# Kernel tuning notes

Measured on AMD Instinct MI355X. Metric: run time of the kernel, lower is better.

## Reference

```python
import jax, jax.numpy as jnp
import numpy as np
import math

D_MODEL = 256
N_LEVELS = 4
N_HEADS = 8
N_POINTS = 4
SPATIAL = [[92, 160], [46, 80], [23, 40], [12, 20]]  # (H_l, W_l)
BATCH = 8
LEN_Q = 8192


def setup_inputs() -> dict:
    key = jax.random.key(0)
    ks = jax.random.split(key, 8)
    len_in = sum(h * w for h, w in SPATIAL)
    query = jax.random.normal(ks[0], (BATCH, LEN_Q, D_MODEL), jnp.float32)
    reference_points = jax.random.uniform(ks[1], (BATCH, LEN_Q, N_LEVELS, 2), jnp.float32)
    input_flatten = jax.random.normal(ks[2], (BATCH, len_in, D_MODEL), jnp.float32)
    input_spatial_shapes = jnp.array(SPATIAL, jnp.int32)
    starts = np.cumsum([0] + [h * w for h, w in SPATIAL])[:-1]
    input_level_start_index = jnp.array(starts, jnp.int32)
    # learned params (sampling_offsets bias uses the directional grid init from _reset_parameters)
    W_off = jax.random.normal(ks[3], (D_MODEL, N_HEADS * N_LEVELS * N_POINTS * 2), jnp.float32) * 0.01
    thetas = jnp.arange(N_HEADS, dtype=jnp.float32) * (2.0 * math.pi / N_HEADS)
    grid = jnp.stack([jnp.cos(thetas), jnp.sin(thetas)], -1)
    grid = grid / jnp.max(jnp.abs(grid), axis=-1, keepdims=True)
    grid = jnp.tile(grid[:, None, None, :], (1, N_LEVELS, N_POINTS, 1))
    grid = grid * jnp.arange(1, N_POINTS + 1, dtype=jnp.float32)[None, None, :, None]
    b_off = grid.reshape(-1)
    W_attn = jax.random.normal(ks[4], (D_MODEL, N_HEADS * N_LEVELS * N_POINTS), jnp.float32) * 0.02
    b_attn = jnp.zeros((N_HEADS * N_LEVELS * N_POINTS,), jnp.float32)
    W_val = jax.random.normal(ks[5], (D_MODEL, D_MODEL), jnp.float32) * (1.0 / math.sqrt(D_MODEL))
    b_val = jnp.zeros((D_MODEL,), jnp.float32)
    W_out = jax.random.normal(ks[6], (D_MODEL, D_MODEL), jnp.float32) * (1.0 / math.sqrt(D_MODEL))
    b_out = jnp.zeros((D_MODEL,), jnp.float32)
    return dict(query=query, reference_points=reference_points, input_flatten=input_flatten,
                input_spatial_shapes=input_spatial_shapes,
                input_level_start_index=input_level_start_index,
                W_off=W_off, b_off=b_off, W_attn=W_attn, b_attn=b_attn,
                W_val=W_val, b_val=b_val, W_out=W_out, b_out=b_out)


def _ms_deform_attn(query, reference_points, input_flatten, spatial_shapes_np,
                    W_off, b_off, W_attn, b_attn, W_val, b_val, W_out, b_out):
    Nb, Lq, C = query.shape
    Hh, L, P = N_HEADS, N_LEVELS, N_POINTS
    Dh = C // Hh
    value = (input_flatten @ W_val + b_val).reshape(Nb, -1, Hh, Dh)
    attn = (query @ W_attn + b_attn).reshape(Nb, Lq, Hh, L * P)
    attn = jax.nn.softmax(attn, axis=-1).reshape(Nb, Lq, Hh, L, P)
    off = (query @ W_off + b_off).reshape(Nb, Lq, Hh, L, P, 2)
    # offset_normalizer = (W_l, H_l)
    norm = jnp.asarray(np.stack([spatial_shapes_np[:, 1], spatial_shapes_np[:, 0]], -1),
                       dtype=query.dtype)  # (L, 2)
    loc = reference_points[:, :, None, :, None, :] + off / norm[None, None, None, :, None, :]
    out = jnp.zeros((Nb, Lq, Hh, Dh), query.dtype)
    start = 0
    for l in range(L):
        H, W = int(spatial_shapes_np[l, 0]), int(spatial_shapes_np[l, 1])
        v = value[:, start:start + H * W]                       # (Nb, H*W, Hh, Dh)
        start += H * W
        v = v.transpose(0, 2, 1, 3).reshape(Nb * Hh, H * W, Dh)  # (B2, H*W, Dh)
        g = loc[:, :, :, l].transpose(0, 2, 1, 3, 4).reshape(Nb * Hh, Lq * P, 2)
        # grid_sample with grid = 2*loc-1, align_corners=False, zero padding
        x = g[..., 0] * W - 0.5
        y = g[..., 1] * H - 0.5
        x0f = jnp.floor(x); y0f = jnp.floor(y)
        wx = x - x0f; wy = y - y0f
        x0 = x0f.astype(jnp.int32); y0 = y0f.astype(jnp.int32)

        def gather(xi, yi):
            valid = (xi >= 0) & (xi < W) & (yi >= 0) & (yi < H)
            idx = jnp.clip(yi, 0, H - 1) * W + jnp.clip(xi, 0, W - 1)
            samp = jnp.take_along_axis(v, idx[..., None], axis=1)  # (B2, Lq*P, Dh)
            return samp * valid[..., None].astype(v.dtype)

        s = (gather(x0, y0) * ((1 - wx) * (1 - wy))[..., None]
             + gather(x0 + 1, y0) * (wx * (1 - wy))[..., None]
             + gather(x0, y0 + 1) * ((1 - wx) * wy)[..., None]
             + gather(x0 + 1, y0 + 1) * (wx * wy)[..., None])
        s = s.reshape(Nb, Hh, Lq, P, Dh)
        w = attn[:, :, :, l].transpose(0, 2, 1, 3)  # (Nb, Hh, Lq, P)
        out = out + jnp.einsum('bhqp,bhqpd->bqhd', w, s)
    return out.reshape(Nb, Lq, C) @ W_out + b_out


def reference(query, reference_points, input_flatten, input_spatial_shapes,
              input_level_start_index, W_off, b_off, W_attn, b_attn,
              W_val, b_val, W_out, b_out):
    # spatial shapes are static metadata (define per-level view sizes)
    shapes_np = np.asarray(input_spatial_shapes)
    del input_level_start_index  # levels are contiguous; starts derived from shapes
    return _ms_deform_attn(query, reference_points, input_flatten, shapes_np,
                           W_off, b_off, W_attn, b_attn, W_val, b_val, W_out, b_out)
```

## Files before the change

### kernel.cpp

```cpp
#include <hip/hip_runtime.h>
#include <hip/hip_bf16.h>
#include <cstddef>
#include <cstdint>

#define NB 8
#define LQ 8192
#define DMODEL 256
#define NHD 8
#define NLV 4
#define NPT 4
#define LEN_IN 19560
#define NQ (NB * LQ)
#define MV (NB * LEN_IN)
#define MVP 156544

using bf16x8 = __attribute__((ext_vector_type(8))) short;
using f32x4  = __attribute__((ext_vector_type(4))) float;

typedef const __attribute__((address_space(1))) void* gas_ptr;
typedef __attribute__((address_space(3))) void* las_ptr;

__device__ __forceinline__ void gl_lds16(const void* g, void* l) {
  __builtin_amdgcn_global_load_lds((gas_ptr)g, (las_ptr)l, 16, 0, 0);
}
__device__ __forceinline__ float bflo(unsigned u) {
  union { unsigned i; float f; } c; c.i = u << 16; return c.f;
}
__device__ __forceinline__ float bfhi(unsigned u) {
  union { unsigned i; float f; } c; c.i = u & 0xffff0000u; return c.f;
}
__device__ __forceinline__ bf16x8 pack8(float4 a, float4 b) {
  bf16x8 o;
  o[0] = (short)__bfloat16_as_ushort(__float2bfloat16(a.x));
  o[1] = (short)__bfloat16_as_ushort(__float2bfloat16(a.y));
  o[2] = (short)__bfloat16_as_ushort(__float2bfloat16(a.z));
  o[3] = (short)__bfloat16_as_ushort(__float2bfloat16(a.w));
  o[4] = (short)__bfloat16_as_ushort(__float2bfloat16(b.x));
  o[5] = (short)__bfloat16_as_ushort(__float2bfloat16(b.y));
  o[6] = (short)__bfloat16_as_ushort(__float2bfloat16(b.z));
  o[7] = (short)__bfloat16_as_ushort(__float2bfloat16(b.w));
  return o;
}

__global__ __launch_bounds__(256) void transpose_bf16(
    const float* __restrict__ W, __hip_bfloat16* __restrict__ Bt, int N) {
  const int o = blockIdx.x * 256 + threadIdx.x;
  const int n = o >> 8, k = o & 255;
  Bt[o] = __float2bfloat16(W[(size_t)k * N + n]);
}

template <int OUT_MODE, int A_F32>
__global__ __launch_bounds__(256) void gemm_mfma(
    const void* __restrict__ Av, const __hip_bfloat16* __restrict__ Bt,
    const float* __restrict__ bias, const float* __restrict__ bias2,
    void* __restrict__ Cout, void* __restrict__ Cout2, int N, int M_valid) {
  __shared__ __hip_bfloat16 As[128 * 32];
  __shared__ __hip_bfloat16 Bs[128 * 32];

  const int tid = threadIdx.x;
  const int wv = tid >> 6;
  const int lane = tid & 63;
  const int quad = lane >> 4;
  const int l16 = lane & 15;
  const int bm = blockIdx.y * 128;
  const int bn = blockIdx.x * 128;
  const int rw = (wv & 1) * 64;
  const int cw = (wv >> 1) * 64;

  const __hip_bfloat16* gB = Bt + (size_t)(bn + (tid >> 2)) * 256 + (tid & 3) * 8;
  char* ldsB0 = (char*)Bs + wv * 1024;

  const __hip_bfloat16* gA16 = nullptr;
  const float* gA32 = nullptr;
  char* ldsA0 = (char*)As + wv * 1024;
  __hip_bfloat16* dA = nullptr;
  bool okA = true;
  if (A_F32) {
    const int r = tid >> 1, half = tid & 1;
    okA = (bm + r) < M_valid;
    gA32 = (const float*)Av + (size_t)(bm + r) * 256 + half * 16;
    dA = As + r * 32 + half * 16;
  } else {
    gA16 = (const __hip_bfloat16*)Av + (size_t)(bm + (tid >> 2)) * 256 +
           (tid & 3) * 8;
  }

  f32x4 acc[4][4] = {};

#pragma unroll 1
  for (int k0 = 0; k0 < 256; k0 += 32) {
    float4 f0, f1, f2, f3;
    if (A_F32) {
      if (okA) {
        f0 = *(const float4*)(gA32 + k0);
        f1 = *(const float4*)(gA32 + k0 + 4);
        f2 = *(const float4*)(gA32 + k0 + 8);
        f3 = *(const float4*)(gA32 + k0 + 12);
      } else {
        f0 = f1 = f2 = f3 = make_float4(0.f, 0.f, 0.f, 0.f);
      }
    }
    __syncthreads();
    gl_lds16(gB + k0, ldsB0);
    gl_lds16(gB + 64 * 256 + k0, ldsB0 + 4096);
    if (A_F32) {
      *(bf16x8*)dA = pack8(f0, f1);
      *(bf16x8*)(dA + 8) = pack8(f2, f3);
    } else {
      gl_lds16(gA16 + k0, ldsA0);
      gl_lds16(gA16 + 64 * 256 + k0, ldsA0 + 4096);
    }
    __syncthreads();

    bf16x8 af[4], bfr[4];
#pragma unroll
    for (int t = 0; t < 4; ++t) {
      af[t] = *(const bf16x8*)(As + (rw + t * 16 + l16) * 32 + quad * 8);
      bfr[t] = *(const bf16x8*)(Bs + (cw + t * 16 + l16) * 32 + quad * 8);
    }
#pragma unroll
    for (int i = 0; i < 4; ++i)
#pragma unroll
      for (int j = 0; j < 4; ++j)
        acc[i][j] = __builtin_amdgcn_mfma_f32_16x16x32_bf16(af[i], bfr[j],
                                                            acc[i][j], 0, 0, 0);
  }

#pragma unroll
  for (int j = 0; j < 4; ++j) {
    const int col = bn + cw + j * 16 + l16;
    float bb;
    if (OUT_MODE == 3)
      bb = (bn == 0) ? bias[col] : bias2[col - 128];
    else
      bb = bias[col];
#pragma unroll
    for (int i = 0; i < 4; ++i) {
#pragma unroll
      for (int r = 0; r < 4; ++r) {
        const int row = bm + rw + i * 16 + quad * 4 + r;
        const float v = acc[i][j][r] + bb;
        if (OUT_MODE == 0) {
          ((float*)Cout)[(size_t)row * N + col] = v;
        } else if (OUT_MODE == 2) {
          if (row < M_valid) {
            const int b = row / LEN_IN;
            const int pix = row - b * LEN_IN;
            const int h = col >> 5, ch = col & 31;
            ((__hip_bfloat16*)Cout)[(((size_t)(b * 8 + h) * LEN_IN + pix) << 5) +
                                    ch] = __float2bfloat16(v);
          }
        } else {
          if (bn == 0) {
            ((float*)Cout)[(size_t)row * 128 + col] = v;
          } else {
            ((__hip_bfloat16*)Cout2)[(size_t)row * 256 + (col - 128)] =
                __float2bfloat16(v);
          }
        }
      }
    }
  }
}

__global__ __launch_bounds__(256) void msda_sample4(
    const float* __restrict__ refp,
    const float* __restrict__ logits,
    const __hip_bfloat16* __restrict__ offb,
    const __hip_bfloat16* __restrict__ vh,
    __hip_bfloat16* __restrict__ mid) {
  const int q0 = blockIdx.x * 2;
  const int tid = threadIdx.x;

  __shared__ int2 s_d[2][8][17][4];

  {
    const int sq = tid >> 7;
    const int t = tid & 127;
    const int qg = q0 + sq;
    const int l = (t >> 2) & 3;
    constexpr int Hs[4] = {92, 46, 23, 12};
    constexpr int Ws_[4] = {160, 80, 40, 20};
    constexpr int St[4] = {0, 14720, 18400, 19320};
    const int Hl = Hs[l], Wl = Ws_[l];

    const float lg = logits[(size_t)qg * 128 + t];
    float mx = lg;
#pragma unroll
    for (int d = 1; d < 16; d <<= 1) mx = fmaxf(mx, __shfl_xor(mx, d));
    const float e = expf(lg - mx);
    float sm = e;
#pragma unroll
    for (int d = 1; d < 16; d <<= 1) sm += __shfl_xor(sm, d);
    const float w = e / sm;

    const float rx = refp[(size_t)qg * 8 + 2 * l];
    const float ry = refp[(size_t)qg * 8 + 2 * l + 1];
    const unsigned uo = *(const unsigned*)(offb + (size_t)qg * 256 + 2 * t);
    const float ox = bflo(uo), oy = bfhi(uo);

    const float x = rx * (float)Wl + ox - 0.5f;
    const float y = ry * (float)Hl + oy - 0.5f;
    const float xf = floorf(x), yf = floorf(y);
    const float wx = x - xf, wy = y - yf;
    const int x0 = (int)xf, y0 = (int)yf;
    const int x1 = x0 + 1, y1 = y0 + 1;
    const bool vx0 = (x0 >= 0) & (x0 < Wl), vx1 = (x1 >= 0) & (x1 < Wl);
    const bool vy0 = (y0 >= 0) & (y0 < Hl), vy1 = (y1 >= 0) & (y1 < Hl);
    const int cx0 = min(max(x0, 0), Wl - 1), cx1 = min(max(x1, 0), Wl - 1);
    const int cy0 = min(max(y0, 0), Hl - 1), cy1 = min(max(y1, 0), Hl - 1);

    const int o00 = (St[l] + cy0 * Wl + cx0) * 64;
    const int o01 = (St[l] + cy1 * Wl + cx0) * 64;
    const int dx = (cx1 - cx0) * 64;

    int2* dd = s_d[sq][t >> 4][t & 15];
    dd[0] = make_int2(o00,      __float_as_int((vx0 & vy0) ? w * (1.f - wx) * (1.f - wy) : 0.f));
    dd[1] = make_int2(o00 + dx, __float_as_int((vx1 & vy0) ? w * wx * (1.f - wy) : 0.f));
    dd[2] = make_int2(o01,      __float_as_int((vx0 & vy1) ? w * (1.f - wx) * wy : 0.f));
    dd[3] = make_int2(o01 + dx, __float_as_int((vx1 & vy1) ? w * wx * wy : 0.f));
  }
  __syncthreads();

  const int tap = tid & 3;
  const int cg = (tid >> 2) & 3;
  const int h = (tid >> 4) & 7;
  const int sq = tid >> 7;
  const int qg = q0 + sq;
  const int bq = q0 >> 13;

  const char* vbase = (const char*)vh + (size_t)bq * (8ULL * LEN_IN * 64);
  const int voff0 = h * (LEN_IN * 64) + cg * 16;
  const int2* sd = &s_d[sq][h][0][tap];

  float a[8] = {};
#pragma unroll
  for (int pt = 0; pt < 16; ++pt) {
    const int2 dw = sd[pt * 4];
    const float w = __int_as_float(dw.y);
    const unsigned voff = (unsigned)(voff0 + dw.x);
    const uint4 u = *(const uint4*)(vbase + voff);
    a[0] += w * bflo(u.x); a[1] += w * bfhi(u.x);
    a[2] += w * bflo(u.y); a[3] += w * bfhi(u.y);
    a[4] += w * bflo(u.z); a[5] += w * bfhi(u.z);
    a[6] += w * bflo(u.w); a[7] += w * bfhi(u.w);
  }

#pragma unroll
  for (int i = 0; i < 8; ++i) a[i] += __shfl_xor(a[i], 1);
#pragma unroll
  for (int i = 0; i < 8; ++i) a[i] += __shfl_xor(a[i], 2);

  if (tap == 0) {
    unsigned short* mp =
        (unsigned short*)mid + (size_t)qg * 256 + h * 32 + cg * 8;
    int4 o;
    o.x = (int)((unsigned)__bfloat16_as_ushort(__float2bfloat16(a[0])) |
                ((unsigned)__bfloat16_as_ushort(__float2bfloat16(a[1])) << 16));
    o.y = (int)((unsigned)__bfloat16_as_ushort(__float2bfloat16(a[2])) |
                ((unsigned)__bfloat16_as_ushort(__float2bfloat16(a[3])) << 16));
    o.z = (int)((unsigned)__bfloat16_as_ushort(__float2bfloat16(a[4])) |
                ((unsigned)__bfloat16_as_ushort(__float2bfloat16(a[5])) << 16));
    o.w = (int)((unsigned)__bfloat16_as_ushort(__float2bfloat16(a[6])) |
                ((unsigned)__bfloat16_as_ushort(__float2bfloat16(a[7])) << 16));
    *(int4*)mp = o;
  }
}

extern "C" void kernel_launch(void* const* d_in, const int* in_sizes, int n_in,
                              void* d_out, int out_size, void* d_ws,
                              size_t ws_size, hipStream_t stream) {
  const float* query = (const float*)d_in[0];
  const float* refp = (const float*)d_in[1];
  const float* inflat = (const float*)d_in[2];
  const float* W_off = (const float*)d_in[5];
  const float* b_off = (const float*)d_in[6];
  const float* W_attn = (const float*)d_in[7];
  const float* b_attn = (const float*)d_in[8];
  const float* W_val = (const float*)d_in[9];
  const float* b_val = (const float*)d_in[10];
  const float* W_out = (const float*)d_in[11];
  const float* b_out = (const float*)d_in[12];
  float* out = (float*)d_out;

  char* ws = (char*)d_ws;
  __hip_bfloat16* vh = (__hip_bfloat16*)(ws);
  float* logits = (float*)(ws + 80117760ULL);
  __hip_bfloat16* offb = (__hip_bfloat16*)(ws + 113672192ULL);
  __hip_bfloat16* mid = (__hip_bfloat16*)(ws + 147226624ULL);
  __hip_bfloat16* Btv = (__hip_bfloat16*)(ws + 180781056ULL);
  __hip_bfloat16* Btc = (__hip_bfloat16*)(ws + 180912128ULL);
  __hip_bfloat16* Btw = (__hip_bfloat16*)(ws + 181108736ULL);

  transpose_bf16<<<256, 256, 0, stream>>>(W_val, Btv, 256);
  transpose_bf16<<<128, 256, 0, stream>>>(W_attn, Btc, 128);
  transpose_bf16<<<256, 256, 0, stream>>>(W_off, Btc + 128 * 256, 256);
  transpose_bf16<<<256, 256, 0, stream>>>(W_out, Btw, 256);

  gemm_mfma<2, 1><<<dim3(2, MVP / 128), 256, 0, stream>>>(
      inflat, Btv, b_val, nullptr, vh, nullptr, 256, MV);
  gemm_mfma<3, 1><<<dim3(3, NQ / 128), 256, 0, stream>>>(
      query, Btc, b_attn, b_off, logits, offb, 384, NQ);
  msda_sample4<<<NQ / 2, 256, 0, stream>>>(refp, logits, offb, vh, mid);
  gemm_mfma<0, 0><<<dim3(2, NQ / 128), 256, 0, stream>>>(
      mid, Btw, b_out, nullptr, out, nullptr, 256, NQ);
}
```

Measured before the change: 575.0 us.

## Double-buffer GEMM LDS tiles and software-pipeline sampler gathers

The MFMA GEMM now keeps two LDS buffers per operand, so the global loads for the next K tile are issued before the current tile's MFMAs run. This hides load latency and drops one barrier per K step. The sampling kernel issues its value gathers in groups of four and prefetches the next group while accumulating the current one, to expose more memory-level parallelism. In exchange, LDS use doubles and register pressure rises, which can lower occupancy.

```diff
diff --git a/kernel.cpp b/kernel.cpp
--- a/kernel.cpp
+++ b/kernel.cpp
@@ -54,8 +54,8 @@
     const void* __restrict__ Av, const __hip_bfloat16* __restrict__ Bt,
     const float* __restrict__ bias, const float* __restrict__ bias2,
     void* __restrict__ Cout, void* __restrict__ Cout2, int N, int M_valid) {
-  __shared__ __hip_bfloat16 As[128 * 32];
-  __shared__ __hip_bfloat16 Bs[128 * 32];
+  __shared__ __hip_bfloat16 As[2][128 * 32];
+  __shared__ __hip_bfloat16 Bs[2][128 * 32];
 
   const int tid = threadIdx.x;
   const int wv = tid >> 6;
@@ -68,18 +68,18 @@
   const int cw = (wv >> 1) * 64;
 
   const __hip_bfloat16* gB = Bt + (size_t)(bn + (tid >> 2)) * 256 + (tid & 3) * 8;
-  char* ldsB0 = (char*)Bs + wv * 1024;
+  char* ldsB0 = (char*)&Bs[0][0] + wv * 1024;
 
   const __hip_bfloat16* gA16 = nullptr;
   const float* gA32 = nullptr;
-  char* ldsA0 = (char*)As + wv * 1024;
+  char* ldsA0 = (char*)&As[0][0] + wv * 1024;
   __hip_bfloat16* dA = nullptr;
   bool okA = true;
   if (A_F32) {
     const int r = tid >> 1, half = tid & 1;
     okA = (bm + r) < M_valid;
     gA32 = (const float*)Av + (size_t)(bm + r) * 256 + half * 16;
-    dA = As + r * 32 + half * 16;
+    dA = &As[0][0] + r * 32 + half * 16;
   } else {
     gA16 = (const __hip_bfloat16*)Av + (size_t)(bm + (tid >> 2)) * 256 +
            (tid & 3) * 8;
@@ -87,44 +87,87 @@
 
   f32x4 acc[4][4] = {};
 
+#define GL_B(t, buf)                                          \
+  do {                                                        \
+    gl_lds16(gB + (t) * 32, ldsB0 + (buf) * 8192);            \
+    gl_lds16(gB + 64 * 256 + (t) * 32,                        \
+             ldsB0 + (buf) * 8192 + 4096);                    \
+  } while (0)
+#define GL_A16(t, buf)                                        \
+  do {                                                        \
+    gl_lds16(gA16 + (t) * 32, ldsA0 + (buf) * 8192);          \
+    gl_lds16(gA16 + 64 * 256 + (t) * 32,                      \
+             ldsA0 + (buf) * 8192 + 4096);                    \
+  } while (0)
+#define LOADA32(t, f)                                         \
+  do {                                                        \
+    if (okA) {                                                \
+      f[0] = *(const float4*)(gA32 + (t) * 32);               \
+      f[1] = *(const float4*)(gA32 + (t) * 32 + 4);           \
+      f[2] = *(const float4*)(gA32 + (t) * 32 + 8);           \
+      f[3] = *(const float4*)(gA32 + (t) * 32 + 12);          \
+    } else {                                                  \
+      f[0] = f[1] = f[2] = f[3] = make_float4(0, 0, 0, 0);    \
+    }                                                         \
+  } while (0)
+#define PACKA(buf, f)                                         \
+  do {                                                        \
+    *(bf16x8*)(dA + (buf) * 4096) = pack8(f[0], f[1]);        \
+    *(bf16x8*)(dA + (buf) * 4096 + 8) = pack8(f[2], f[3]);    \
+  } while (0)
+#define COMPUTE(buf)                                                        \
+  do {                                                                      \
+    bf16x8 af[4], bfr[4];                                                   \
+    _Pragma("unroll") for (int t = 0; t < 4; ++t) {                         \
+      af[t] = *(const bf16x8*)(&As[0][0] + (buf) * 4096 +                   \
+                               (rw + t * 16 + l16) * 32 + quad * 8);        \
+      bfr[t] = *(const bf16x8*)(&Bs[0][0] + (buf) * 4096 +                  \
+                                (cw + t * 16 + l16) * 32 + quad * 8);       \
+    }                                                                       \
+    _Pragma("unroll") for (int i = 0; i < 4; ++i)                           \
+        _Pragma("unroll") for (int j = 0; j < 4; ++j) acc[i][j] =           \
+        __builtin_amdgcn_mfma_f32_16x16x32_bf16(af[i], bfr[j], acc[i][j],   \
+                                                0, 0, 0);                   \
+  } while (0)
+
+  {
+    float4 f[4];
+    if (A_F32) LOADA32(0, f);
+    GL_B(0, 0);
+    if (!A_F32) GL_A16(0, 0);
+    if (A_F32) PACKA(0, f);
+  }
+  __syncthreads();
+
 #pragma unroll 1
-  for (int k0 = 0; k0 < 256; k0 += 32) {
-    float4 f0, f1, f2, f3;
-    if (A_F32) {
-      if (okA) {
-        f0 = *(const float4*)(gA32 + k0);
-        f1 = *(const float4*)(gA32 + k0 + 4);
-        f2 = *(const float4*)(gA32 + k0 + 8);
-        f3 = *(const float4*)(gA32 + k0 + 12);
-      } else {
-        f0 = f1 = f2 = f3 = make_float4(0.f, 0.f, 0.f, 0.f);
-      }
+  for (int tt = 0; tt < 4; ++tt) {
+    {
+      float4 fb[4];
+      if (A_F32) LOADA32(2 * tt + 1, fb);
+      GL_B(2 * tt + 1, 1);
+      if (!A_F32) GL_A16(2 * tt + 1, 1);
+      COMPUTE(0);
+      if (A_F32) PACKA(1, fb);
     }
     __syncthreads();
-    gl_lds16(gB + k0, ldsB0);
-    gl_lds16(gB + 64 * 256 + k0, ldsB0 + 4096);
-    if (A_F32) {
-      *(bf16x8*)dA = pack8(f0, f1);
-      *(bf16x8*)(dA + 8) = pack8(f2, f3);
+    if (tt < 3) {
+      float4 fc[4];
+      if (A_F32) LOADA32(2 * tt + 2, fc);
+      GL_B(2 * tt + 2, 0);
+      if (!A_F32) GL_A16(2 * tt + 2, 0);
+      COMPUTE(1);
+      if (A_F32) PACKA(0, fc);
     } else {
-      gl_lds16(gA16 + k0, ldsA0);
-      gl_lds16(gA16 + 64 * 256 + k0, ldsA0 + 4096);
+      COMPUTE(1);
     }
     __syncthreads();
-
-    bf16x8 af[4], bfr[4];
-#pragma unroll
-    for (int t = 0; t < 4; ++t) {
-      af[t] = *(const bf16x8*)(As + (rw + t * 16 + l16) * 32 + quad * 8);
-      bfr[t] = *(const bf16x8*)(Bs + (cw + t * 16 + l16) * 32 + quad * 8);
-    }
-#pragma unroll
-    for (int i = 0; i < 4; ++i)
-#pragma unroll
-      for (int j = 0; j < 4; ++j)
-        acc[i][j] = __builtin_amdgcn_mfma_f32_16x16x32_bf16(af[i], bfr[j],
-                                                            acc[i][j], 0, 0, 0);
-  }
+  }
+
+#undef GL_B
+#undef GL_A16
+#undef LOADA32
+#undef PACKA
+#undef COMPUTE
 
 #pragma unroll
   for (int j = 0; j < 4; ++j) {
@@ -163,7 +206,7 @@
   }
 }
 
-__global__ __launch_bounds__(256) void msda_sample4(
+__global__ __launch_bounds__(256) void msda_sample5(
     const float* __restrict__ refp,
     const float* __restrict__ logits,
     const __hip_bfloat16* __restrict__ offb,
@@ -234,16 +277,41 @@
   const int2* sd = &s_d[sq][h][0][tap];
 
   float a[8] = {};
-#pragma unroll
-  for (int pt = 0; pt < 16; ++pt) {
-    const int2 dw = sd[pt * 4];
-    const float w = __int_as_float(dw.y);
-    const unsigned voff = (unsigned)(voff0 + dw.x);
-    const uint4 u = *(const uint4*)(vbase + voff);
-    a[0] += w * bflo(u.x); a[1] += w * bfhi(u.x);
-    a[2] += w * bflo(u.y); a[3] += w * bfhi(u.y);
-    a[4] += w * bflo(u.z); a[5] += w * bfhi(u.z);
-    a[6] += w * bflo(u.w); a[7] += w * bfhi(u.w);
+  int2 d[4];
+  uint4 u[4];
+#pragma unroll
+  for (int j = 0; j < 4; ++j) d[j] = sd[j * 4];
+#pragma unroll
+  for (int j = 0; j < 4; ++j)
+    u[j] = *(const uint4*)(vbase + (unsigned)(voff0 + d[j].x));
+
+#pragma unroll
+  for (int g = 0; g < 4; ++g) {
+    int2 dn[4];
+    uint4 un[4];
+    if (g < 3) {
+#pragma unroll
+      for (int j = 0; j < 4; ++j) dn[j] = sd[(g * 4 + 4 + j) * 4];
+#pragma unroll
+      for (int j = 0; j < 4; ++j)
+        un[j] = *(const uint4*)(vbase + (unsigned)(voff0 + dn[j].x));
+    }
+#pragma unroll
+    for (int j = 0; j < 4; ++j) {
+      const float w = __int_as_float(d[j].y);
+      const uint4 uu = u[j];
+      a[0] += w * bflo(uu.x); a[1] += w * bfhi(uu.x);
+      a[2] += w * bflo(uu.y); a[3] += w * bfhi(uu.y);
+      a[4] += w * bflo(uu.z); a[5] += w * bfhi(uu.z);
+      a[6] += w * bflo(uu.w); a[7] += w * bfhi(uu.w);
+    }
+    if (g < 3) {
+#pragma unroll
+      for (int j = 0; j < 4; ++j) {
+        d[j] = dn[j];
+        u[j] = un[j];
+      }
+    }
   }
 
 #pragma unroll
@@ -301,7 +369,7 @@
       inflat, Btv, b_val, nullptr, vh, nullptr, 256, MV);
   gemm_mfma<3, 1><<<dim3(3, NQ / 128), 256, 0, stream>>>(
       query, Btc, b_attn, b_off, logits, offb, 384, NQ);
-  msda_sample4<<<NQ / 2, 256, 0, stream>>>(refp, logits, offb, vh, mid);
+  msda_sample5<<<NQ / 2, 256, 0, stream>>>(refp, logits, offb, vh, mid);
   gemm_mfma<0, 0><<<dim3(2, NQ / 128), 256, 0, stream>>>(
       mid, Btw, b_out, nullptr, out, nullptr, 256, NQ);
 }
```

After: 587.4 us. 2.1% more time.

## Widen GEMM tiles to full N per block and batch gathers in sampler

Applied to the files above, without the earlier changes.

Each GEMM block now covers the whole output width (256 or 384 columns) with 512 threads, so each fp32 A tile is loaded and converted to bf16 once instead of once per column block. The sampling kernel issues all 16 value gathers into registers before accumulating, which exposes more memory-level parallelism, and it gets a launch-bounds occupancy hint. In exchange the GEMM grid is smaller and each block holds more accumulators, and the sampler needs more registers for the staged loads.

```diff
diff --git a/kernel.cpp b/kernel.cpp
--- a/kernel.cpp
+++ b/kernel.cpp
@@ -49,89 +49,86 @@
   Bt[o] = __float2bfloat16(W[(size_t)k * N + n]);
 }
 
-template <int OUT_MODE, int A_F32>
-__global__ __launch_bounds__(256) void gemm_mfma(
+template <int OUT_MODE, int A_F32, int NT>
+__global__ __launch_bounds__(512) void gemm_mfma(
     const void* __restrict__ Av, const __hip_bfloat16* __restrict__ Bt,
     const float* __restrict__ bias, const float* __restrict__ bias2,
-    void* __restrict__ Cout, void* __restrict__ Cout2, int N, int M_valid) {
+    void* __restrict__ Cout, void* __restrict__ Cout2, int M_valid) {
+  constexpr int NJ = NT / 64;
   __shared__ __hip_bfloat16 As[128 * 32];
-  __shared__ __hip_bfloat16 Bs[128 * 32];
+  __shared__ __hip_bfloat16 Bs[NT * 32];
 
   const int tid = threadIdx.x;
   const int wv = tid >> 6;
   const int lane = tid & 63;
   const int quad = lane >> 4;
   const int l16 = lane & 15;
-  const int bm = blockIdx.y * 128;
-  const int bn = blockIdx.x * 128;
+  const int bm = blockIdx.x * 128;
   const int rw = (wv & 1) * 64;
-  const int cw = (wv >> 1) * 64;
-
-  const __hip_bfloat16* gB = Bt + (size_t)(bn + (tid >> 2)) * 256 + (tid & 3) * 8;
-  char* ldsB0 = (char*)Bs + wv * 1024;
+  const int cwave = (wv >> 1) * (NT / 4);
+
+  const __hip_bfloat16* gB = Bt + (size_t)(tid >> 2) * 256 + (tid & 3) * 8;
 
   const __hip_bfloat16* gA16 = nullptr;
   const float* gA32 = nullptr;
-  char* ldsA0 = (char*)As + wv * 1024;
   __hip_bfloat16* dA = nullptr;
   bool okA = true;
   if (A_F32) {
-    const int r = tid >> 1, half = tid & 1;
+    const int r = tid >> 2, seg = tid & 3;
     okA = (bm + r) < M_valid;
-    gA32 = (const float*)Av + (size_t)(bm + r) * 256 + half * 16;
-    dA = As + r * 32 + half * 16;
+    gA32 = (const float*)Av + (size_t)(bm + r) * 256 + seg * 8;
+    dA = As + r * 32 + seg * 8;
   } else {
     gA16 = (const __hip_bfloat16*)Av + (size_t)(bm + (tid >> 2)) * 256 +
            (tid & 3) * 8;
   }
 
-  f32x4 acc[4][4] = {};
+  f32x4 acc[4][NJ] = {};
 
 #pragma unroll 1
   for (int k0 = 0; k0 < 256; k0 += 32) {
-    float4 f0, f1, f2, f3;
+    float4 f0, f1;
     if (A_F32) {
       if (okA) {
         f0 = *(const float4*)(gA32 + k0);
         f1 = *(const float4*)(gA32 + k0 + 4);
-        f2 = *(const float4*)(gA32 + k0 + 8);
-        f3 = *(const float4*)(gA32 + k0 + 12);
       } else {
-        f0 = f1 = f2 = f3 = make_float4(0.f, 0.f, 0.f, 0.f);
+        f0 = f1 = make_float4(0.f, 0.f, 0.f, 0.f);
       }
     }
     __syncthreads();
-    gl_lds16(gB + k0, ldsB0);
-    gl_lds16(gB + 64 * 256 + k0, ldsB0 + 4096);
+#pragma unroll
+    for (int c = 0; c < NT / 128; ++c)
+      gl_lds16(gB + (size_t)c * 128 * 256 + k0,
+               (char*)Bs + c * 8192 + wv * 1024);
     if (A_F32) {
       *(bf16x8*)dA = pack8(f0, f1);
-      *(bf16x8*)(dA + 8) = pack8(f2, f3);
     } else {
-      gl_lds16(gA16 + k0, ldsA0);
-      gl_lds16(gA16 + 64 * 256 + k0, ldsA0 + 4096);
+      gl_lds16(gA16 + k0, (char*)As + wv * 1024);
     }
     __syncthreads();
 
-    bf16x8 af[4], bfr[4];
-#pragma unroll
-    for (int t = 0; t < 4; ++t) {
+    bf16x8 af[4], bfr[NJ];
+#pragma unroll
+    for (int t = 0; t < 4; ++t)
       af[t] = *(const bf16x8*)(As + (rw + t * 16 + l16) * 32 + quad * 8);
-      bfr[t] = *(const bf16x8*)(Bs + (cw + t * 16 + l16) * 32 + quad * 8);
-    }
+#pragma unroll
+    for (int j = 0; j < NJ; ++j)
+      bfr[j] = *(const bf16x8*)(Bs + (cwave + j * 16 + l16) * 32 + quad * 8);
 #pragma unroll
     for (int i = 0; i < 4; ++i)
 #pragma unroll
-      for (int j = 0; j < 4; ++j)
+      for (int j = 0; j < NJ; ++j)
         acc[i][j] = __builtin_amdgcn_mfma_f32_16x16x32_bf16(af[i], bfr[j],
                                                             acc[i][j], 0, 0, 0);
   }
 
 #pragma unroll
-  for (int j = 0; j < 4; ++j) {
-    const int col = bn + cw + j * 16 + l16;
+  for (int j = 0; j < NJ; ++j) {
+    const int col = cwave + j * 16 + l16;
     float bb;
     if (OUT_MODE == 3)
-      bb = (bn == 0) ? bias[col] : bias2[col - 128];
+      bb = (col < 128) ? bias[col] : bias2[col - 128];
     else
       bb = bias[col];
 #pragma unroll
@@ -141,7 +138,7 @@
         const int row = bm + rw + i * 16 + quad * 4 + r;
         const float v = acc[i][j][r] + bb;
         if (OUT_MODE == 0) {
-          ((float*)Cout)[(size_t)row * N + col] = v;
+          ((float*)Cout)[(size_t)row * NT + col] = v;
         } else if (OUT_MODE == 2) {
           if (row < M_valid) {
             const int b = row / LEN_IN;
@@ -151,7 +148,7 @@
                                     ch] = __float2bfloat16(v);
           }
         } else {
-          if (bn == 0) {
+          if (col < 128) {
             ((float*)Cout)[(size_t)row * 128 + col] = v;
           } else {
             ((__hip_bfloat16*)Cout2)[(size_t)row * 256 + (col - 128)] =
@@ -163,7 +160,7 @@
   }
 }
 
-__global__ __launch_bounds__(256) void msda_sample4(
+__global__ __launch_bounds__(256, 4) void msda_sample6(
     const float* __restrict__ refp,
     const float* __restrict__ logits,
     const __hip_bfloat16* __restrict__ offb,
@@ -233,17 +230,22 @@
   const int voff0 = h * (LEN_IN * 64) + cg * 16;
   const int2* sd = &s_d[sq][h][0][tap];
 
+  float w[16];
+  uint4 u[16];
+#pragma unroll
+  for (int j = 0; j < 16; ++j) {
+    const int2 dw = sd[j * 4];
+    w[j] = __int_as_float(dw.y);
+    u[j] = *(const uint4*)(vbase + (unsigned)(voff0 + dw.x));
+  }
+
   float a[8] = {};
 #pragma unroll
-  for (int pt = 0; pt < 16; ++pt) {
-    const int2 dw = sd[pt * 4];
-    const float w = __int_as_float(dw.y);
-    const unsigned voff = (unsigned)(voff0 + dw.x);
-    const uint4 u = *(const uint4*)(vbase + voff);
-    a[0] += w * bflo(u.x); a[1] += w * bfhi(u.x);
-    a[2] += w * bflo(u.y); a[3] += w * bfhi(u.y);
-    a[4] += w * bflo(u.z); a[5] += w * bfhi(u.z);
-    a[6] += w * bflo(u.w); a[7] += w * bfhi(u.w);
+  for (int j = 0; j < 16; ++j) {
+    a[0] += w[j] * bflo(u[j].x); a[1] += w[j] * bfhi(u[j].x);
+    a[2] += w[j] * bflo(u[j].y); a[3] += w[j] * bfhi(u[j].y);
+    a[4] += w[j] * bflo(u[j].z); a[5] += w[j] * bfhi(u[j].z);
+    a[6] += w[j] * bflo(u[j].w); a[7] += w[j] * bfhi(u[j].w);
   }
 
 #pragma unroll
@@ -297,11 +299,11 @@
   transpose_bf16<<<256, 256, 0, stream>>>(W_off, Btc + 128 * 256, 256);
   transpose_bf16<<<256, 256, 0, stream>>>(W_out, Btw, 256);
 
-  gemm_mfma<2, 1><<<dim3(2, MVP / 128), 256, 0, stream>>>(
-      inflat, Btv, b_val, nullptr, vh, nullptr, 256, MV);
-  gemm_mfma<3, 1><<<dim3(3, NQ / 128), 256, 0, stream>>>(
-      query, Btc, b_attn, b_off, logits, offb, 384, NQ);
-  msda_sample4<<<NQ / 2, 256, 0, stream>>>(refp, logits, offb, vh, mid);
-  gemm_mfma<0, 0><<<dim3(2, NQ / 128), 256, 0, stream>>>(
-      mid, Btw, b_out, nullptr, out, nullptr, 256, NQ);
-}
+  gemm_mfma<2, 1, 256><<<MVP / 128, 512, 0, stream>>>(
+      inflat, Btv, b_val, nullptr, vh, nullptr, MV);
+  gemm_mfma<3, 1, 384><<<NQ / 128, 512, 0, stream>>>(
+      query, Btc, b_attn, b_off, logits, offb, NQ);
+  msda_sample6<<<NQ / 2, 256, 0, stream>>>(refp, logits, offb, vh, mid);
+  gemm_mfma<0, 0, 256><<<NQ / 128, 512, 0, stream>>>(
+      mid, Btw, b_out, nullptr, out, nullptr, NQ);
+}
```

New measurement: 530.1 us. 1.08x faster.
